# Kernel optimization log

Measured on AMD Instinct MI355X. Metric: run time of the kernel, lower is better.

The kernel has to match this reference:

```python
import jax, jax.numpy as jnp
import numpy as np

N = 50000       # nodes
E = 150000      # directed edges
NODE_IN = 64
EDGE_IN = 16
D = 32          # node_out_feats
EDGE_HID = 128
STEPS = 3       # num_step_message_passing


def setup_inputs() -> dict:
    key = jax.random.key(0)
    ks = jax.random.split(key, 10)
    s = 0.05
    return {
        "x": jax.random.normal(ks[0], (N, NODE_IN), jnp.float32),
        "edge_index": jax.random.randint(ks[1], (2, E), 0, N),
        "edge_attr": jax.random.normal(ks[2], (E, EDGE_IN), jnp.float32),
        # node_init Linear
        "Wn": jax.random.normal(ks[3], (NODE_IN, D), jnp.float32) * s,
        "bn": jnp.zeros((D,), jnp.float32),
        # edge_network: Linear(edge_in, hid) -> ReLU -> Linear(hid, D*D)
        "We1": jax.random.normal(ks[4], (EDGE_IN, EDGE_HID), jnp.float32) * s,
        "be1": jnp.zeros((EDGE_HID,), jnp.float32),
        "We2": jax.random.normal(ks[5], (EDGE_HID, D * D), jnp.float32) * s,
        "be2": jnp.zeros((D * D,), jnp.float32),
        # NNConv root weight + bias
        "Wroot": jax.random.normal(ks[6], (D, D), jnp.float32) * s,
        "bconv": jnp.zeros((D,), jnp.float32),
        # GRU (gate order r, z, n as in torch)
        "Wih": jax.random.normal(ks[7], (3 * D, D), jnp.float32) * s,
        "Whh": jax.random.normal(ks[8], (3 * D, D), jnp.float32) * s,
        "bih": jnp.zeros((3 * D,), jnp.float32),
        "bhh": jnp.zeros((3 * D,), jnp.float32),
    }


def _gru_cell(xt, h, Wih, Whh, bih, bhh):
    gi = xt @ Wih.T + bih   # [N, 3D]
    gh = h @ Whh.T + bhh    # [N, 3D]
    r = jax.nn.sigmoid(gi[:, :D] + gh[:, :D])
    z = jax.nn.sigmoid(gi[:, D:2 * D] + gh[:, D:2 * D])
    n = jnp.tanh(gi[:, 2 * D:] + r * gh[:, 2 * D:])
    return (1.0 - z) * n + z * h


def reference(x, edge_index, edge_attr, Wn, bn, We1, be1, We2, be2,
              Wroot, bconv, Wih, Whh, bih, bhh):
    src, dst = edge_index[0], edge_index[1]
    # per-edge weight matrices from edge_network (edge_attr fixed across steps)
    Wm = (jax.nn.relu(edge_attr @ We1 + be1) @ We2 + be2).reshape(E, D, D)
    h = jax.nn.relu(x @ Wn + bn)   # node_init
    hid = h                        # GRU hidden state
    for _ in range(STEPS):
        # NNConv: gather -> per-edge matmul -> scatter-add, plus root + bias
        m = jnp.einsum('ei,eio->eo', h[src], Wm)                # [E, D]
        agg = jax.ops.segment_sum(m, dst, num_segments=N)       # [N, D]
        conv = jax.nn.relu(agg + h @ Wroot + bconv)
        hid = _gru_cell(conv, hid, Wih, Whh, bih, bhh)
        h = hid
    return h
```

## Files before the change

### kernel.cpp

```cpp
#include <hip/hip_runtime.h>
#include <hip/hip_bf16.h>

#define N_NODES 50000
#define N_EDGES 150000
#define NODE_IN 64
#define EDGE_IN 16
#define DD 32
#define EHID 128
#define STEPS 3
#define EPB 128
#define NSCAN 196

__device__ __forceinline__ ushort f2b(float f) {
    __hip_bfloat16 b = __float2bfloat16(f);
    return *reinterpret_cast<ushort*>(&b);
}
__device__ __forceinline__ float b2f(ushort u) {
    unsigned int x = ((unsigned int)u) << 16;
    return __uint_as_float(x);
}

typedef __bf16 bf16x8 __attribute__((ext_vector_type(8)));
typedef float  f32x4  __attribute__((ext_vector_type(4)));

#define LDA  136
#define HPAD 36
#define MPAD 40

__global__ __launch_bounds__(256) void prep(const float* __restrict__ we2,
                                            const float* __restrict__ we1,
                                            const float* __restrict__ wroot,
                                            const float* __restrict__ wih,
                                            const float* __restrict__ whh,
                                            ushort* __restrict__ we2B,
                                            ushort* __restrict__ we1B,
                                            ushort* __restrict__ wgB) {
    int i = blockIdx.x * 256 + threadIdx.x;
    if (i < 16384) {
        int l = i & 63, f = i >> 6;
        int kt = f & 3, nt = (f >> 2) & 3, bn = f >> 4;
        int lr = l & 15, lg = l >> 4;
        int n = bn * 64 + nt * 16 + lr;
        int k0 = kt * 32 + lg * 8;
        ushort tmp[8];
#pragma unroll
        for (int j = 0; j < 8; ++j) tmp[j] = f2b(we2[(size_t)(k0 + j) * 1024 + n]);
        *(uint4*)(we2B + (size_t)i * 8) = *(uint4*)tmp;
    } else if (i < 16896) {
        int u = i - 16384;
        int l = u & 63, nt = u >> 6;
        int lr = l & 15, lg = l >> 4;
        int n = nt * 16 + lr;
        ushort tmp[8];
#pragma unroll
        for (int j = 0; j < 8; ++j) {
            int k = lg * 8 + j;
            tmp[j] = (k < EDGE_IN) ? f2b(we1[(size_t)k * EHID + n]) : (ushort)0;
        }
        *(uint4*)(we1B + (size_t)u * 8) = *(uint4*)tmp;
    } else if (i < 17792) {
        int u = i - 16896;
        int l = u & 63;
        int lr = l & 15, lg = l >> 4;
        ushort tmp[8];
        if (u < 128) {
            int nt = u >> 6;
#pragma unroll
            for (int j = 0; j < 8; ++j)
                tmp[j] = f2b(wroot[(size_t)(lg * 8 + j) * DD + nt * 16 + lr]);
        } else if (u < 512) {
            int nt = (u - 128) >> 6;
#pragma unroll
            for (int j = 0; j < 8; ++j)
                tmp[j] = f2b(wih[(size_t)(nt * 16 + lr) * DD + lg * 8 + j]);
        } else {
            int nt = (u - 512) >> 6;
#pragma unroll
            for (int j = 0; j < 8; ++j)
                tmp[j] = f2b(whh[(size_t)(nt * 16 + lr) * DD + lg * 8 + j]);
        }
        *(uint4*)(wgB + (size_t)u * 8) = *(uint4*)tmp;
    }
}

__global__ __launch_bounds__(256) void hist(const int* __restrict__ ei,
                                            int* __restrict__ cnt) {
    int e = blockIdx.x * 256 + threadIdx.x;
    if (e < N_EDGES) atomicAdd(&cnt[ei[N_EDGES + e]], 1);
}

__global__ __launch_bounds__(256) void scan1(int* __restrict__ cnt,
                                             int* __restrict__ bsum) {
    __shared__ int wsum[4];
    int b = blockIdx.x, t = threadIdx.x;
    int lane = t & 63, wid = t >> 6;
    int i = b * 256 + t;
    int v = (i < N_NODES) ? cnt[i] : 0;
    int s = v;
#pragma unroll
    for (int off = 1; off < 64; off <<= 1) {
        int u = __shfl_up(s, off);
        if (lane >= off) s += u;
    }
    if (lane == 63) wsum[wid] = s;
    __syncthreads();
    if (t == 0) {
        int a = 0;
#pragma unroll
        for (int k = 0; k < 4; ++k) { int tmp = wsum[k]; wsum[k] = a; a += tmp; }
    }
    __syncthreads();
    int excl = s - v + wsum[wid];
    if (i < N_NODES) cnt[i] = excl;
    if (t == 255) bsum[b] = excl + v;
}

__global__ __launch_bounds__(256) void scan2(int* __restrict__ bsum) {
    __shared__ int wsum[4];
    int t = threadIdx.x;
    int lane = t & 63, wid = t >> 6;
    int v = (t < NSCAN) ? bsum[t] : 0;
    int s = v;
#pragma unroll
    for (int off = 1; off < 64; off <<= 1) {
        int u = __shfl_up(s, off);
        if (lane >= off) s += u;
    }
    if (lane == 63) wsum[wid] = s;
    __syncthreads();
    if (t == 0) {
        int a = 0;
#pragma unroll
        for (int k = 0; k < 4; ++k) { int tmp = wsum[k]; wsum[k] = a; a += tmp; }
    }
    __syncthreads();
    if (t < NSCAN) bsum[t] = s - v + wsum[wid];
}

__global__ __launch_bounds__(256) void scan3(const int* __restrict__ cnt,
                                             const int* __restrict__ bsum,
                                             int* __restrict__ off,
                                             int* __restrict__ cur) {
    int i = blockIdx.x * 256 + threadIdx.x;
    if (i < N_NODES) {
        int o = cnt[i] + bsum[blockIdx.x];
        off[i] = o;
        cur[i] = o;
    }
}

__global__ __launch_bounds__(256) void scatter_fill(const int* __restrict__ ei,
                                                    int* __restrict__ cur,
                                                    int* __restrict__ perm,
                                                    int* __restrict__ srcs) {
    int e = blockIdx.x * 256 + threadIdx.x;
    if (e >= N_EDGES) return;
    int d = ei[N_EDGES + e];
    int pos = atomicAdd(&cur[d], 1);
    perm[pos] = e;
    srcs[pos] = ei[e];
}

__global__ __launch_bounds__(256) void node_init(const float* __restrict__ x,
                                                 const float* __restrict__ Wn,
                                                 const float* __restrict__ bn,
                                                 float* __restrict__ h) {
    __shared__ float Wns[NODE_IN * DD];
    __shared__ float bns[DD];
    int t = threadIdx.x;
    for (int i = t; i < NODE_IN * DD; i += 256) Wns[i] = Wn[i];
    if (t < DD) bns[t] = bn[t];
    __syncthreads();
    int n = blockIdx.x * 256 + t;
    if (n >= N_NODES) return;
    float xr[NODE_IN];
    const float4* xp = (const float4*)(x + (size_t)n * NODE_IN);
#pragma unroll
    for (int q = 0; q < NODE_IN / 4; ++q) *(float4*)&xr[q * 4] = xp[q];
    float out[DD];
#pragma unroll
    for (int o = 0; o < DD; ++o) {
        float s = bns[o];
#pragma unroll
        for (int i = 0; i < NODE_IN; ++i) s += xr[i] * Wns[i * DD + o];
        out[o] = fmaxf(s, 0.f);
    }
    float4* hp = (float4*)(h + (size_t)n * DD);
#pragma unroll
    for (int q = 0; q < DD / 4; ++q) hp[q] = *(float4*)&out[q * 4];
}

__global__ __launch_bounds__(256, 4) void fused_msg(const float* __restrict__ ea,
                                                    const ushort* __restrict__ we1B,
                                                    const float* __restrict__ be1,
                                                    const ushort* __restrict__ we2B,
                                                    const float* __restrict__ be2,
                                                    const int* __restrict__ perm,
                                                    const int* __restrict__ srcs,
                                                    const float* __restrict__ h,
                                                    ushort* __restrict__ msg) {
    __shared__ __attribute__((aligned(16))) ushort AsHs[EPB * LDA];
    __shared__ float b1s[EHID];
    __shared__ float be2s[DD * DD];
    float* Hs = (float*)AsHs;
    ushort* Bs = AsHs + 9216;
    ushort* Ms = AsHs;

    int t = threadIdx.x;
    if (t < EHID) b1s[t] = be1[t];
    for (int i = t; i < DD * DD; i += 256) be2s[i] = be2[i];

    int w = t >> 6, l = t & 63;
    int lr = l & 15, lg = l >> 4;
    int e0 = blockIdx.x * EPB;

    bf16x8 afe[2];
#pragma unroll
    for (int mi = 0; mi < 2; ++mi) {
        int e = e0 + (w * 2 + mi) * 16 + lr;
        ushort tmp[8] = {0, 0, 0, 0, 0, 0, 0, 0};
        if (lg < 2 && e < N_EDGES) {
            int pe = perm[e];
            const float4* p = (const float4*)(ea + (size_t)pe * EDGE_IN + lg * 8);
            float4 a = p[0], b = p[1];
            tmp[0] = f2b(a.x); tmp[1] = f2b(a.y); tmp[2] = f2b(a.z); tmp[3] = f2b(a.w);
            tmp[4] = f2b(b.x); tmp[5] = f2b(b.y); tmp[6] = f2b(b.z); tmp[7] = f2b(b.w);
        }
        afe[mi] = *(bf16x8*)tmp;
    }
    __syncthreads();

#pragma unroll
    for (int nt = 0; nt < 8; ++nt) {
        bf16x8 bfe = *(const bf16x8*)(we1B + (size_t)((nt << 6) + l) * 8);
        int kh = nt * 16 + lr;
        float bb = b1s[kh];
#pragma unroll
        for (int mi = 0; mi < 2; ++mi) {
            f32x4 acc = (f32x4){0.f, 0.f, 0.f, 0.f};
            acc = __builtin_amdgcn_mfma_f32_16x16x32_bf16(afe[mi], bfe, acc, 0, 0, 0);
#pragma unroll
            for (int r = 0; r < 4; ++r)
                AsHs[((w * 2 + mi) * 16 + lg * 4 + r) * LDA + kh] = f2b(fmaxf(acc[r] + bb, 0.f));
        }
    }
    __syncthreads();

    bf16x8 afrag[2][4];
#pragma unroll
    for (int mi = 0; mi < 2; ++mi)
#pragma unroll
        for (int kt = 0; kt < 4; ++kt)
            afrag[mi][kt] = *(const bf16x8*)(&AsHs[((w * 2 + mi) * 16 + lr) * LDA + kt * 32 + lg * 8]);
    __syncthreads();

    {
        int row = t >> 1, half = t & 1;
        int e = e0 + row;
        float4* hd = (float4*)(Hs + row * HPAD) + half * 4;
        if (e < N_EDGES) {
            const float4* hr = (const float4*)(h + (size_t)srcs[e] * DD) + half * 4;
#pragma unroll
            for (int q = 0; q < 4; ++q) hd[q] = hr[q];
        } else {
            float4 z = make_float4(0.f, 0.f, 0.f, 0.f);
#pragma unroll
            for (int q = 0; q < 4; ++q) hd[q] = z;
        }
    }
#pragma unroll
    for (int q = 0; q < 4; ++q) {
        const ushort* gsrc = we2B + (size_t)(q * 256 + t) * 8;
        ushort* ldst = Bs + (size_t)(q * 256 + w * 64) * 8;
        __builtin_amdgcn_global_load_lds(
            (const __attribute__((address_space(1))) unsigned int*)gsrc,
            (__attribute__((address_space(3))) unsigned int*)ldst, 16, 0, 0);
    }
    asm volatile("s_waitcnt vmcnt(0)" ::: "memory");
    __syncthreads();

    float m_acc[2][4][2];
#pragma unroll
    for (int mi = 0; mi < 2; ++mi)
#pragma unroll
        for (int r = 0; r < 4; ++r) { m_acc[mi][r][0] = 0.f; m_acc[mi][r][1] = 0.f; }

    for (int bn = 0; bn < 16; ++bn) {
        float bv[4];
#pragma unroll
        for (int nt = 0; nt < 4; ++nt) bv[nt] = be2s[bn * 64 + nt * 16 + lr];

        f32x4 acc[2][4];
#pragma unroll
        for (int mi = 0; mi < 2; ++mi)
#pragma unroll
            for (int nt = 0; nt < 4; ++nt) acc[mi][nt] = (f32x4){0.f, 0.f, 0.f, 0.f};

#pragma unroll
        for (int kt = 0; kt < 4; ++kt) {
            const ushort* base = Bs + (size_t)(kt * 64 + l) * 8;
            bf16x8 b0 = *(const bf16x8*)(base);
            bf16x8 b1 = *(const bf16x8*)(base + 2048);
            bf16x8 b2 = *(const bf16x8*)(base + 4096);
            bf16x8 b3 = *(const bf16x8*)(base + 6144);
#pragma unroll
            for (int mi = 0; mi < 2; ++mi) {
                acc[mi][0] = __builtin_amdgcn_mfma_f32_16x16x32_bf16(afrag[mi][kt], b0, acc[mi][0], 0, 0, 0);
                acc[mi][1] = __builtin_amdgcn_mfma_f32_16x16x32_bf16(afrag[mi][kt], b1, acc[mi][1], 0, 0, 0);
                acc[mi][2] = __builtin_amdgcn_mfma_f32_16x16x32_bf16(afrag[mi][kt], b2, acc[mi][2], 0, 0, 0);
                acc[mi][3] = __builtin_amdgcn_mfma_f32_16x16x32_bf16(afrag[mi][kt], b3, acc[mi][3], 0, 0, 0);
            }
        }

#pragma unroll
        for (int mi = 0; mi < 2; ++mi) {
#pragma unroll
            for (int r = 0; r < 4; ++r) {
                int row = (w * 2 + mi) * 16 + lg * 4 + r;
                float2 hv = *(const float2*)(Hs + row * HPAD + bn * 2);
#pragma unroll
                for (int nt = 0; nt < 4; ++nt) {
                    float hi = (nt >> 1) ? hv.y : hv.x;
                    m_acc[mi][r][nt & 1] += hi * (acc[mi][nt][r] + bv[nt]);
                }
            }
        }

        if (bn < 15) {
            __syncthreads();
#pragma unroll
            for (int q = 0; q < 4; ++q) {
                const ushort* gsrc = we2B + (size_t)(bn + 1) * 8192 + (size_t)(q * 256 + t) * 8;
                ushort* ldst = Bs + (size_t)(q * 256 + w * 64) * 8;
                __builtin_amdgcn_global_load_lds(
                    (const __attribute__((address_space(1))) unsigned int*)gsrc,
                    (__attribute__((address_space(3))) unsigned int*)ldst, 16, 0, 0);
            }
            asm volatile("s_waitcnt vmcnt(0)" ::: "memory");
            __syncthreads();
        }
    }

    __syncthreads();
#pragma unroll
    for (int mi = 0; mi < 2; ++mi) {
#pragma unroll
        for (int r = 0; r < 4; ++r) {
            int row = (w * 2 + mi) * 16 + lg * 4 + r;
            Ms[row * MPAD + lr]      = f2b(m_acc[mi][r][0]);
            Ms[row * MPAD + lr + 16] = f2b(m_acc[mi][r][1]);
        }
    }
    __syncthreads();
    {
        int row = t >> 1, half = t & 1;
        int e = e0 + row;
        if (e < N_EDGES) {
            const uint4* src = (const uint4*)(Ms + row * MPAD);
            uint4* dst = (uint4*)(msg + (size_t)e * DD);
            dst[half * 2]     = src[half * 2];
            dst[half * 2 + 1] = src[half * 2 + 1];
        }
    }
}

__global__ __launch_bounds__(256) void conv_gru(const ushort* __restrict__ msg,
                                                const int* __restrict__ off,
                                                float* __restrict__ h,
                                                const ushort* __restrict__ wgB,
                                                const float* __restrict__ bconv,
                                                const float* __restrict__ bih,
                                                const float* __restrict__ bhh) {
    __shared__ __attribute__((aligned(16))) ushort Ah[64 * 40];
    __shared__ __attribute__((aligned(16))) ushort Ac[64 * 40];
    __shared__ float hs[64 * 33];
    __shared__ float bcs[DD], bis[3 * DD], bhs[3 * DD];
    int t = threadIdx.x;
    int base = blockIdx.x * 64;

    for (int idx = t; idx < 64 * DD; idx += 256) {
        int row = idx >> 5, col = idx & 31;
        int n = base + row;
        float v = (n < N_NODES) ? h[(size_t)n * DD + col] : 0.f;
        hs[row * 33 + col] = v;
        Ah[row * 40 + col] = f2b(v);
    }
    if (t < DD) bcs[t] = bconv[t];
    if (t < 3 * DD) { bis[t] = bih[t]; bhs[t] = bhh[t]; }
    __syncthreads();

    int w = t >> 6, l = t & 63;
    int lr = l & 15, lg = l >> 4;
    const f32x4 zro = (f32x4){0.f, 0.f, 0.f, 0.f};

    bf16x8 ah = *(const bf16x8*)(&Ah[(w * 16 + lr) * 40 + lg * 8]);

    f32x4 dcv[2];
#pragma unroll
    for (int nt = 0; nt < 2; ++nt) {
        bf16x8 b = *(const bf16x8*)(wgB + (size_t)(nt * 64 + l) * 8);
        dcv[nt] = __builtin_amdgcn_mfma_f32_16x16x32_bf16(ah, b, zro, 0, 0, 0);
    }
#pragma unroll
    for (int r = 0; r < 4; ++r) {
        int row = w * 16 + lg * 4 + r;
        int n = base + row;
        float a0 = 0.f, a1 = 0.f;
        if (n < N_NODES) {
            int beg = off[n];
            int end = (n + 1 < N_NODES) ? off[n + 1] : N_EDGES;
            for (int j = beg; j < end; ++j) {
                const ushort* mr = msg + (size_t)j * DD;
                a0 += b2f(mr[lr]);
                a1 += b2f(mr[lr + 16]);
            }
        }
        Ac[row * 40 + lr]      = f2b(fmaxf(dcv[0][r] + a0 + bcs[lr], 0.f));
        Ac[row * 40 + lr + 16] = f2b(fmaxf(dcv[1][r] + a1 + bcs[lr + 16], 0.f));
    }
    __syncthreads();

    bf16x8 ac = *(const bf16x8*)(&Ac[(w * 16 + lr) * 40 + lg * 8]);

    f32x4 gi[6], gh[6];
#pragma unroll
    for (int nt = 0; nt < 6; ++nt) {
        bf16x8 bi_ = *(const bf16x8*)(wgB + (size_t)(128 + nt * 64 + l) * 8);
        gi[nt] = __builtin_amdgcn_mfma_f32_16x16x32_bf16(ac, bi_, zro, 0, 0, 0);
        bf16x8 bh_ = *(const bf16x8*)(wgB + (size_t)(512 + nt * 64 + l) * 8);
        gh[nt] = __builtin_amdgcn_mfma_f32_16x16x32_bf16(ah, bh_, zro, 0, 0, 0);
    }

#pragma unroll
    for (int r = 0; r < 4; ++r) {
        int row = w * 16 + lg * 4 + r;
        int n = base + row;
        if (n >= N_NODES) continue;
#pragma unroll
        for (int ch = 0; ch < 2; ++ch) {
            int o = ch * 16 + lr;
            float girv = gi[ch][r]     + bis[o];
            float gizv = gi[2 + ch][r] + bis[DD + o];
            float ginv = gi[4 + ch][r] + bis[2 * DD + o];
            float ghrv = gh[ch][r]     + bhs[o];
            float ghzv = gh[2 + ch][r] + bhs[DD + o];
            float ghnv = gh[4 + ch][r] + bhs[2 * DD + o];
            float R  = 1.f / (1.f + expf(-(girv + ghrv)));
            float Z  = 1.f / (1.f + expf(-(gizv + ghzv)));
            float Nn = tanhf(ginv + R * ghnv);
            float hold = hs[row * 33 + o];
            float hnew = (1.f - Z) * Nn + Z * hold;
            h[(size_t)n * DD + o] = hnew;
        }
    }
}

extern "C" void kernel_launch(void* const* d_in, const int* in_sizes, int n_in,
                              void* d_out, int out_size, void* d_ws, size_t ws_size,
                              hipStream_t stream) {
    const float* x    = (const float*)d_in[0];
    const int*   ei   = (const int*)d_in[1];
    const float* ea   = (const float*)d_in[2];
    const float* Wn   = (const float*)d_in[3];
    const float* bn   = (const float*)d_in[4];
    const float* We1  = (const float*)d_in[5];
    const float* be1  = (const float*)d_in[6];
    const float* We2  = (const float*)d_in[7];
    const float* be2  = (const float*)d_in[8];
    const float* Wroot= (const float*)d_in[9];
    const float* bconv= (const float*)d_in[10];
    const float* Wih  = (const float*)d_in[11];
    const float* Whh  = (const float*)d_in[12];
    const float* bih  = (const float*)d_in[13];
    const float* bhh  = (const float*)d_in[14];

    char* ws = (char*)d_ws;
    ushort* msg  = (ushort*)(ws);
    ushort* we2B = (ushort*)(ws + 9600000);
    ushort* we1B = (ushort*)(ws + 9862144);
    ushort* wgB  = (ushort*)(ws + 9870336);
    int*    cnt  = (int*)(ws + 9884672);
    int*    off  = (int*)(ws + 10084672);
    int*    cur  = (int*)(ws + 10284672);
    int*    perm = (int*)(ws + 10484672);
    int*    srcs = (int*)(ws + 11084672);
    int*    bsum = (int*)(ws + 11684672);
    float*  h    = (float*)d_out;

    hipMemsetAsync(cnt, 0, (size_t)N_NODES * sizeof(int), stream);
    prep<<<70, 256, 0, stream>>>(We2, We1, Wroot, Wih, Whh, we2B, we1B, wgB);
    node_init<<<(N_NODES + 255) / 256, 256, 0, stream>>>(x, Wn, bn, h);
    hist<<<(N_EDGES + 255) / 256, 256, 0, stream>>>(ei, cnt);
    scan1<<<NSCAN, 256, 0, stream>>>(cnt, bsum);
    scan2<<<1, 256, 0, stream>>>(bsum);
    scan3<<<NSCAN, 256, 0, stream>>>(cnt, bsum, off, cur);
    scatter_fill<<<(N_EDGES + 255) / 256, 256, 0, stream>>>(ei, cur, perm, srcs);

    for (int step = 0; step < STEPS; ++step) {
        fused_msg<<<(N_EDGES + EPB - 1) / EPB, 256, 0, stream>>>(ea, we1B, be1, we2B, be2,
                                                                 perm, srcs, h, msg);
        conv_gru<<<(N_NODES + 63) / 64, 256, 0, stream>>>(msg, off, h, wgB,
                                                          bconv, bih, bhh);
    }
}
```

Measured before the change: 354.2 us.

## Merge setup kernels, halve edges per message block, stage messages in LDS

```diff
diff --git a/kernel.cpp b/kernel.cpp
--- a/kernel.cpp
+++ b/kernel.cpp
@@ -8,8 +8,9 @@
 #define DD 32
 #define EHID 128
 #define STEPS 3
-#define EPB 128
+#define EPB 64
 #define NSCAN 196
+#define MGCAP 384
 
 __device__ __forceinline__ ushort f2b(float f) {
     __hip_bfloat16 b = __float2bfloat16(f);
@@ -27,66 +28,96 @@
 #define HPAD 36
 #define MPAD 40
 
-__global__ __launch_bounds__(256) void prep(const float* __restrict__ we2,
-                                            const float* __restrict__ we1,
-                                            const float* __restrict__ wroot,
-                                            const float* __restrict__ wih,
-                                            const float* __restrict__ whh,
-                                            ushort* __restrict__ we2B,
-                                            ushort* __restrict__ we1B,
-                                            ushort* __restrict__ wgB) {
-    int i = blockIdx.x * 256 + threadIdx.x;
-    if (i < 16384) {
-        int l = i & 63, f = i >> 6;
-        int kt = f & 3, nt = (f >> 2) & 3, bn = f >> 4;
-        int lr = l & 15, lg = l >> 4;
-        int n = bn * 64 + nt * 16 + lr;
-        int k0 = kt * 32 + lg * 8;
-        ushort tmp[8];
-#pragma unroll
-        for (int j = 0; j < 8; ++j) tmp[j] = f2b(we2[(size_t)(k0 + j) * 1024 + n]);
-        *(uint4*)(we2B + (size_t)i * 8) = *(uint4*)tmp;
-    } else if (i < 16896) {
-        int u = i - 16384;
-        int l = u & 63, nt = u >> 6;
-        int lr = l & 15, lg = l >> 4;
-        int n = nt * 16 + lr;
-        ushort tmp[8];
-#pragma unroll
-        for (int j = 0; j < 8; ++j) {
-            int k = lg * 8 + j;
-            tmp[j] = (k < EDGE_IN) ? f2b(we1[(size_t)k * EHID + n]) : (ushort)0;
-        }
-        *(uint4*)(we1B + (size_t)u * 8) = *(uint4*)tmp;
-    } else if (i < 17792) {
-        int u = i - 16896;
-        int l = u & 63;
-        int lr = l & 15, lg = l >> 4;
-        ushort tmp[8];
-        if (u < 128) {
-            int nt = u >> 6;
-#pragma unroll
-            for (int j = 0; j < 8; ++j)
-                tmp[j] = f2b(wroot[(size_t)(lg * 8 + j) * DD + nt * 16 + lr]);
-        } else if (u < 512) {
-            int nt = (u - 128) >> 6;
-#pragma unroll
-            for (int j = 0; j < 8; ++j)
-                tmp[j] = f2b(wih[(size_t)(nt * 16 + lr) * DD + lg * 8 + j]);
-        } else {
-            int nt = (u - 512) >> 6;
-#pragma unroll
-            for (int j = 0; j < 8; ++j)
-                tmp[j] = f2b(whh[(size_t)(nt * 16 + lr) * DD + lg * 8 + j]);
-        }
-        *(uint4*)(wgB + (size_t)u * 8) = *(uint4*)tmp;
-    }
-}
-
-__global__ __launch_bounds__(256) void hist(const int* __restrict__ ei,
-                                            int* __restrict__ cnt) {
-    int e = blockIdx.x * 256 + threadIdx.x;
-    if (e < N_EDGES) atomicAdd(&cnt[ei[N_EDGES + e]], 1);
+__global__ __launch_bounds__(256) void setup(const float* __restrict__ we2,
+                                             const float* __restrict__ we1,
+                                             const float* __restrict__ wroot,
+                                             const float* __restrict__ wih,
+                                             const float* __restrict__ whh,
+                                             ushort* __restrict__ we2B,
+                                             ushort* __restrict__ we1B,
+                                             ushort* __restrict__ wgB,
+                                             const float* __restrict__ x,
+                                             const float* __restrict__ Wn,
+                                             const float* __restrict__ bn,
+                                             float* __restrict__ h,
+                                             const int* __restrict__ ei,
+                                             int* __restrict__ cnt) {
+    __shared__ float Wns[NODE_IN * DD];
+    __shared__ float bns[DD];
+    int b = blockIdx.x, t = threadIdx.x;
+
+    if (b < 70) {
+        int i = b * 256 + t;
+        if (i < 16384) {
+            int l = i & 63, f = i >> 6;
+            int kt = f & 3, nt = (f >> 2) & 3, bq = f >> 4;
+            int lr = l & 15, lg = l >> 4;
+            int n = bq * 64 + nt * 16 + lr;
+            int k0 = kt * 32 + lg * 8;
+            ushort tmp[8];
+#pragma unroll
+            for (int j = 0; j < 8; ++j) tmp[j] = f2b(we2[(size_t)(k0 + j) * 1024 + n]);
+            *(uint4*)(we2B + (size_t)i * 8) = *(uint4*)tmp;
+        } else if (i < 16896) {
+            int u = i - 16384;
+            int l = u & 63, nt = u >> 6;
+            int lr = l & 15, lg = l >> 4;
+            int n = nt * 16 + lr;
+            ushort tmp[8];
+#pragma unroll
+            for (int j = 0; j < 8; ++j) {
+                int k = lg * 8 + j;
+                tmp[j] = (k < EDGE_IN) ? f2b(we1[(size_t)k * EHID + n]) : (ushort)0;
+            }
+            *(uint4*)(we1B + (size_t)u * 8) = *(uint4*)tmp;
+        } else if (i < 17792) {
+            int u = i - 16896;
+            int l = u & 63;
+            int lr = l & 15, lg = l >> 4;
+            ushort tmp[8];
+            if (u < 128) {
+                int nt = u >> 6;
+#pragma unroll
+                for (int j = 0; j < 8; ++j)
+                    tmp[j] = f2b(wroot[(size_t)(lg * 8 + j) * DD + nt * 16 + lr]);
+            } else if (u < 512) {
+                int nt = (u - 128) >> 6;
+#pragma unroll
+                for (int j = 0; j < 8; ++j)
+                    tmp[j] = f2b(wih[(size_t)(nt * 16 + lr) * DD + lg * 8 + j]);
+            } else {
+                int nt = (u - 512) >> 6;
+#pragma unroll
+                for (int j = 0; j < 8; ++j)
+                    tmp[j] = f2b(whh[(size_t)(nt * 16 + lr) * DD + lg * 8 + j]);
+            }
+            *(uint4*)(wgB + (size_t)u * 8) = *(uint4*)tmp;
+        }
+    } else if (b < 266) {
+        for (int i = t; i < NODE_IN * DD; i += 256) Wns[i] = Wn[i];
+        if (t < DD) bns[t] = bn[t];
+        __syncthreads();
+        int n = (b - 70) * 256 + t;
+        if (n >= N_NODES) return;
+        float xr[NODE_IN];
+        const float4* xp = (const float4*)(x + (size_t)n * NODE_IN);
+#pragma unroll
+        for (int q = 0; q < NODE_IN / 4; ++q) *(float4*)&xr[q * 4] = xp[q];
+        float out[DD];
+#pragma unroll
+        for (int o = 0; o < DD; ++o) {
+            float s = bns[o];
+#pragma unroll
+            for (int i = 0; i < NODE_IN; ++i) s += xr[i] * Wns[i * DD + o];
+            out[o] = fmaxf(s, 0.f);
+        }
+        float4* hp = (float4*)(h + (size_t)n * DD);
+#pragma unroll
+        for (int q = 0; q < DD / 4; ++q) hp[q] = *(float4*)&out[q * 4];
+    } else {
+        int e = (b - 266) * 256 + t;
+        if (e < N_EDGES) atomicAdd(&cnt[ei[N_EDGES + e]], 1);
+    }
 }
 
 __global__ __launch_bounds__(256) void scan1(int* __restrict__ cnt,
@@ -161,36 +192,7 @@
     srcs[pos] = ei[e];
 }
 
-__global__ __launch_bounds__(256) void node_init(const float* __restrict__ x,
-                                                 const float* __restrict__ Wn,
-                                                 const float* __restrict__ bn,
-                                                 float* __restrict__ h) {
-    __shared__ float Wns[NODE_IN * DD];
-    __shared__ float bns[DD];
-    int t = threadIdx.x;
-    for (int i = t; i < NODE_IN * DD; i += 256) Wns[i] = Wn[i];
-    if (t < DD) bns[t] = bn[t];
-    __syncthreads();
-    int n = blockIdx.x * 256 + t;
-    if (n >= N_NODES) return;
-    float xr[NODE_IN];
-    const float4* xp = (const float4*)(x + (size_t)n * NODE_IN);
-#pragma unroll
-    for (int q = 0; q < NODE_IN / 4; ++q) *(float4*)&xr[q * 4] = xp[q];
-    float out[DD];
-#pragma unroll
-    for (int o = 0; o < DD; ++o) {
-        float s = bns[o];
-#pragma unroll
-        for (int i = 0; i < NODE_IN; ++i) s += xr[i] * Wns[i * DD + o];
-        out[o] = fmaxf(s, 0.f);
-    }
-    float4* hp = (float4*)(h + (size_t)n * DD);
-#pragma unroll
-    for (int q = 0; q < DD / 4; ++q) hp[q] = *(float4*)&out[q * 4];
-}
-
-__global__ __launch_bounds__(256, 4) void fused_msg(const float* __restrict__ ea,
+__global__ __launch_bounds__(256, 5) void fused_msg(const float* __restrict__ ea,
                                                     const ushort* __restrict__ we1B,
                                                     const float* __restrict__ be1,
                                                     const ushort* __restrict__ we2B,
@@ -199,11 +201,11 @@
                                                     const int* __restrict__ srcs,
                                                     const float* __restrict__ h,
                                                     ushort* __restrict__ msg) {
-    __shared__ __attribute__((aligned(16))) ushort AsHs[EPB * LDA];
+    __shared__ __attribute__((aligned(16))) ushort AsHs[12800];
     __shared__ float b1s[EHID];
     __shared__ float be2s[DD * DD];
     float* Hs = (float*)AsHs;
-    ushort* Bs = AsHs + 9216;
+    ushort* Bs = AsHs + 4608;
     ushort* Ms = AsHs;
 
     int t = threadIdx.x;
@@ -214,10 +216,9 @@
     int lr = l & 15, lg = l >> 4;
     int e0 = blockIdx.x * EPB;
 
-    bf16x8 afe[2];
-#pragma unroll
-    for (int mi = 0; mi < 2; ++mi) {
-        int e = e0 + (w * 2 + mi) * 16 + lr;
+    bf16x8 afe;
+    {
+        int e = e0 + w * 16 + lr;
         ushort tmp[8] = {0, 0, 0, 0, 0, 0, 0, 0};
         if (lg < 2 && e < N_EDGES) {
             int pe = perm[e];
@@ -226,7 +227,7 @@
             tmp[0] = f2b(a.x); tmp[1] = f2b(a.y); tmp[2] = f2b(a.z); tmp[3] = f2b(a.w);
             tmp[4] = f2b(b.x); tmp[5] = f2b(b.y); tmp[6] = f2b(b.z); tmp[7] = f2b(b.w);
         }
-        afe[mi] = *(bf16x8*)tmp;
+        afe = *(bf16x8*)tmp;
     }
     __syncthreads();
 
@@ -235,37 +236,31 @@
         bf16x8 bfe = *(const bf16x8*)(we1B + (size_t)((nt << 6) + l) * 8);
         int kh = nt * 16 + lr;
         float bb = b1s[kh];
-#pragma unroll
-        for (int mi = 0; mi < 2; ++mi) {
-            f32x4 acc = (f32x4){0.f, 0.f, 0.f, 0.f};
-            acc = __builtin_amdgcn_mfma_f32_16x16x32_bf16(afe[mi], bfe, acc, 0, 0, 0);
-#pragma unroll
-            for (int r = 0; r < 4; ++r)
-                AsHs[((w * 2 + mi) * 16 + lg * 4 + r) * LDA + kh] = f2b(fmaxf(acc[r] + bb, 0.f));
-        }
-    }
-    __syncthreads();
-
-    bf16x8 afrag[2][4];
-#pragma unroll
-    for (int mi = 0; mi < 2; ++mi)
-#pragma unroll
-        for (int kt = 0; kt < 4; ++kt)
-            afrag[mi][kt] = *(const bf16x8*)(&AsHs[((w * 2 + mi) * 16 + lr) * LDA + kt * 32 + lg * 8]);
+        f32x4 acc = (f32x4){0.f, 0.f, 0.f, 0.f};
+        acc = __builtin_amdgcn_mfma_f32_16x16x32_bf16(afe, bfe, acc, 0, 0, 0);
+#pragma unroll
+        for (int r = 0; r < 4; ++r)
+            AsHs[(w * 16 + lg * 4 + r) * LDA + kh] = f2b(fmaxf(acc[r] + bb, 0.f));
+    }
+    __syncthreads();
+
+    bf16x8 afrag[4];
+#pragma unroll
+    for (int kt = 0; kt < 4; ++kt)
+        afrag[kt] = *(const bf16x8*)(&AsHs[(w * 16 + lr) * LDA + kt * 32 + lg * 8]);
     __syncthreads();
 
     {
-        int row = t >> 1, half = t & 1;
+        int row = t >> 2, qtr = t & 3;
         int e = e0 + row;
-        float4* hd = (float4*)(Hs + row * HPAD) + half * 4;
+        float4* hd = (float4*)(Hs + row * HPAD) + qtr * 2;
         if (e < N_EDGES) {
-            const float4* hr = (const float4*)(h + (size_t)srcs[e] * DD) + half * 4;
-#pragma unroll
-            for (int q = 0; q < 4; ++q) hd[q] = hr[q];
+            const float4* hr = (const float4*)(h + (size_t)srcs[e] * DD) + qtr * 2;
+            hd[0] = hr[0];
+            hd[1] = hr[1];
         } else {
             float4 z = make_float4(0.f, 0.f, 0.f, 0.f);
-#pragma unroll
-            for (int q = 0; q < 4; ++q) hd[q] = z;
+            hd[0] = z; hd[1] = z;
         }
     }
 #pragma unroll
@@ -279,22 +274,18 @@
     asm volatile("s_waitcnt vmcnt(0)" ::: "memory");
     __syncthreads();
 
-    float m_acc[2][4][2];
-#pragma unroll
-    for (int mi = 0; mi < 2; ++mi)
-#pragma unroll
-        for (int r = 0; r < 4; ++r) { m_acc[mi][r][0] = 0.f; m_acc[mi][r][1] = 0.f; }
+    float m_acc[4][2];
+#pragma unroll
+    for (int r = 0; r < 4; ++r) { m_acc[r][0] = 0.f; m_acc[r][1] = 0.f; }
 
     for (int bn = 0; bn < 16; ++bn) {
         float bv[4];
 #pragma unroll
         for (int nt = 0; nt < 4; ++nt) bv[nt] = be2s[bn * 64 + nt * 16 + lr];
 
-        f32x4 acc[2][4];
-#pragma unroll
-        for (int mi = 0; mi < 2; ++mi)
-#pragma unroll
-            for (int nt = 0; nt < 4; ++nt) acc[mi][nt] = (f32x4){0.f, 0.f, 0.f, 0.f};
+        f32x4 acc[4];
+#pragma unroll
+        for (int nt = 0; nt < 4; ++nt) acc[nt] = (f32x4){0.f, 0.f, 0.f, 0.f};
 
 #pragma unroll
         for (int kt = 0; kt < 4; ++kt) {
@@ -303,26 +294,20 @@
             bf16x8 b1 = *(const bf16x8*)(base + 2048);
             bf16x8 b2 = *(const bf16x8*)(base + 4096);
             bf16x8 b3 = *(const bf16x8*)(base + 6144);
-#pragma unroll
-            for (int mi = 0; mi < 2; ++mi) {
-                acc[mi][0] = __builtin_amdgcn_mfma_f32_16x16x32_bf16(afrag[mi][kt], b0, acc[mi][0], 0, 0, 0);
-                acc[mi][1] = __builtin_amdgcn_mfma_f32_16x16x32_bf16(afrag[mi][kt], b1, acc[mi][1], 0, 0, 0);
-                acc[mi][2] = __builtin_amdgcn_mfma_f32_16x16x32_bf16(afrag[mi][kt], b2, acc[mi][2], 0, 0, 0);
-                acc[mi][3] = __builtin_amdgcn_mfma_f32_16x16x32_bf16(afrag[mi][kt], b3, acc[mi][3], 0, 0, 0);
-            }
-        }
-
-#pragma unroll
-        for (int mi = 0; mi < 2; ++mi) {
-#pragma unroll
-            for (int r = 0; r < 4; ++r) {
-                int row = (w * 2 + mi) * 16 + lg * 4 + r;
-                float2 hv = *(const float2*)(Hs + row * HPAD + bn * 2);
-#pragma unroll
-                for (int nt = 0; nt < 4; ++nt) {
-                    float hi = (nt >> 1) ? hv.y : hv.x;
-                    m_acc[mi][r][nt & 1] += hi * (acc[mi][nt][r] + bv[nt]);
-                }
+            acc[0] = __builtin_amdgcn_mfma_f32_16x16x32_bf16(afrag[kt], b0, acc[0], 0, 0, 0);
+            acc[1] = __builtin_amdgcn_mfma_f32_16x16x32_bf16(afrag[kt], b1, acc[1], 0, 0, 0);
+            acc[2] = __builtin_amdgcn_mfma_f32_16x16x32_bf16(afrag[kt], b2, acc[2], 0, 0, 0);
+            acc[3] = __builtin_amdgcn_mfma_f32_16x16x32_bf16(afrag[kt], b3, acc[3], 0, 0, 0);
+        }
+
+#pragma unroll
+        for (int r = 0; r < 4; ++r) {
+            int row = w * 16 + lg * 4 + r;
+            float2 hv = *(const float2*)(Hs + row * HPAD + bn * 2);
+#pragma unroll
+            for (int nt = 0; nt < 4; ++nt) {
+                float hi = (nt >> 1) ? hv.y : hv.x;
+                m_acc[r][nt & 1] += hi * (acc[nt][r] + bv[nt]);
             }
         }
 
@@ -343,23 +328,19 @@
 
     __syncthreads();
 #pragma unroll
-    for (int mi = 0; mi < 2; ++mi) {
-#pragma unroll
-        for (int r = 0; r < 4; ++r) {
-            int row = (w * 2 + mi) * 16 + lg * 4 + r;
-            Ms[row * MPAD + lr]      = f2b(m_acc[mi][r][0]);
-            Ms[row * MPAD + lr + 16] = f2b(m_acc[mi][r][1]);
-        }
+    for (int r = 0; r < 4; ++r) {
+        int row = w * 16 + lg * 4 + r;
+        Ms[row * MPAD + lr]      = f2b(m_acc[r][0]);
+        Ms[row * MPAD + lr + 16] = f2b(m_acc[r][1]);
     }
     __syncthreads();
     {
-        int row = t >> 1, half = t & 1;
+        int row = t >> 2, qtr = t & 3;
         int e = e0 + row;
         if (e < N_EDGES) {
-            const uint4* src = (const uint4*)(Ms + row * MPAD);
-            uint4* dst = (uint4*)(msg + (size_t)e * DD);
-            dst[half * 2]     = src[half * 2];
-            dst[half * 2 + 1] = src[half * 2 + 1];
+            const uint4* src = (const uint4*)(Ms + row * MPAD + qtr * 8);
+            uint4* dst = (uint4*)(msg + (size_t)e * DD + qtr * 8);
+            dst[0] = src[0];
         }
     }
 }
@@ -373,10 +354,19 @@
                                                 const float* __restrict__ bhh) {
     __shared__ __attribute__((aligned(16))) ushort Ah[64 * 40];
     __shared__ __attribute__((aligned(16))) ushort Ac[64 * 40];
+    __shared__ __attribute__((aligned(16))) ushort Mg[MGCAP * DD];
     __shared__ float hs[64 * 33];
     __shared__ float bcs[DD], bis[3 * DD], bhs[3 * DD];
     int t = threadIdx.x;
     int base = blockIdx.x * 64;
+
+    int rowBeg = off[base];
+    int rowEnd = (base + 64 < N_NODES) ? off[base + 64] : N_EDGES;
+    int nrows = rowEnd - rowBeg;
+    int nstage = nrows < MGCAP ? nrows : MGCAP;
+
+    for (int i = t; i < nstage * 4; i += 256)
+        *(uint4*)(Mg + (size_t)i * 8) = *(const uint4*)(msg + (size_t)rowBeg * DD + (size_t)i * 8);
 
     for (int idx = t; idx < 64 * DD; idx += 256) {
         int row = idx >> 5, col = idx & 31;
@@ -407,10 +397,11 @@
         int n = base + row;
         float a0 = 0.f, a1 = 0.f;
         if (n < N_NODES) {
-            int beg = off[n];
-            int end = (n + 1 < N_NODES) ? off[n + 1] : N_EDGES;
-            for (int j = beg; j < end; ++j) {
-                const ushort* mr = msg + (size_t)j * DD;
+            int beg = off[n] - rowBeg;
+            int end2 = ((n + 1 < N_NODES) ? off[n + 1] : N_EDGES) - rowBeg;
+            for (int j = beg; j < end2; ++j) {
+                const ushort* mr = (j < MGCAP) ? (Mg + (size_t)j * DD)
+                                               : (msg + (size_t)(rowBeg + j) * DD);
                 a0 += b2f(mr[lr]);
                 a1 += b2f(mr[lr + 16]);
             }
@@ -488,9 +479,8 @@
     float*  h    = (float*)d_out;
 
     hipMemsetAsync(cnt, 0, (size_t)N_NODES * sizeof(int), stream);
-    prep<<<70, 256, 0, stream>>>(We2, We1, Wroot, Wih, Whh, we2B, we1B, wgB);
-    node_init<<<(N_NODES + 255) / 256, 256, 0, stream>>>(x, Wn, bn, h);
-    hist<<<(N_EDGES + 255) / 256, 256, 0, stream>>>(ei, cnt);
+    setup<<<852, 256, 0, stream>>>(We2, We1, Wroot, Wih, Whh, we2B, we1B, wgB,
+                                   x, Wn, bn, h, ei, cnt);
     scan1<<<NSCAN, 256, 0, stream>>>(cnt, bsum);
     scan2<<<1, 256, 0, stream>>>(bsum);
     scan3<<<NSCAN, 256, 0, stream>>>(cnt, bsum, off, cur);
```

After: 358.2 us. No clear change (+1.1%).
